# Performance work log

Hardware: AMD Instinct MI355X
Metric: run time of the kernel (lower is better)

The kernel has to match this reference:

```python
import jax, jax.numpy as jnp
import numpy as np

B, DIM, H, W = 128, 640, 10, 10
M = H * W


def setup_inputs() -> dict:
    key = jax.random.key(0)
    x = jax.random.normal(key, (B, DIM, M), dtype=jnp.float32)
    # learned temperature parameter, init = log(1 / (2*h*w)), shape (1, 1)
    t = jnp.log(1.0 / (2 * H * W) * jnp.ones((1, 1), dtype=jnp.float32))
    return {"x": x, "t": t}


def reference(x, t):
    # x: [B, dim, M], t: [1, 1] temperature (log-scale)
    dim = x.shape[1]
    # Gram matrix x x^T: [B, dim, dim]
    xxT = jnp.einsum('bdm,bem->bde', x, x)
    # I_M.bmm(x_pow2*I) and (x_pow2*I).bmm(I_M) are just diagonal broadcasts
    d = jnp.diagonal(xxT, axis1=1, axis2=2)  # [B, dim]
    dcov = d[:, None, :] + d[:, :, None] - 2.0 * xxT
    dcov = jnp.maximum(dcov, 1e-4)
    dcov = jnp.sqrt(jnp.exp(t) * dcov + 1e-5)
    # double centering: dcov.bmm(I_M)/dim == row means, I_M.bmm(dcov)/dim == col means
    row_mean = jnp.mean(dcov, axis=2, keepdims=True)   # [B, dim, 1]
    col_mean = jnp.mean(dcov, axis=1, keepdims=True)   # [B, 1, dim]
    tot_mean = jnp.mean(dcov, axis=(1, 2), keepdims=True)  # [B, 1, 1]
    out = dcov - row_mean - col_mean + tot_mean
    return out.reshape(out.shape[0], dim * dim)
```

## Files before the change

### kernel.cpp

```cpp
#include <hip/hip_runtime.h>
#include <cmath>

#define NB    128
#define DIM_  640
#define MM    100
#define LDK   136
#define TS    72
#define TTS   68

#define NWG   (NB * 55)
#define CPX   (NWG / 8)

typedef _Float16 half8 __attribute__((ext_vector_type(8)));
typedef _Float16 half4_t __attribute__((ext_vector_type(4)));
typedef float f32x4 __attribute__((ext_vector_type(4)));

__device__ inline void decode_bp(int bid, int& b, int& p) {
    const int dec = (bid & 7) * CPX + (bid >> 3);
    b = dec / 55;
    p = dec - b * 55;
}

__device__ inline void stage_tile_d(const float* __restrict__ src,
                                    _Float16* __restrict__ lds,
                                    float* __restrict__ dsrow, int tid) {
    const int row = tid >> 2;
    const int sub = tid & 3;
    const float* sr = src + (size_t)row * MM + sub * 4;
    _Float16* lr = lds + row * LDK + sub * 4;
    float acc = 0.f;
    #pragma unroll
    for (int k = 0; k < 6; ++k) {
        const float4 v = *(const float4*)(sr + 16 * k);
        half4_t h;
        h.x = (_Float16)v.x; h.y = (_Float16)v.y;
        h.z = (_Float16)v.z; h.w = (_Float16)v.w;
        *(half4_t*)(lr + 16 * k) = h;
        const float a0 = (float)h.x, a1 = (float)h.y,
                    a2 = (float)h.z, a3 = (float)h.w;
        acc += a0 * a0 + a1 * a1 + a2 * a2 + a3 * a3;
    }
    if (sub == 0) {
        const float4 v = *(const float4*)(sr + 96);
        half4_t h;
        h.x = (_Float16)v.x; h.y = (_Float16)v.y;
        h.z = (_Float16)v.z; h.w = (_Float16)v.w;
        *(half4_t*)(lr + 96) = h;
        const float a0 = (float)h.x, a1 = (float)h.y,
                    a2 = (float)h.z, a3 = (float)h.w;
        acc += a0 * a0 + a1 * a1 + a2 * a2 + a3 * a3;
    }
    acc += __shfl_xor(acc, 1, 64);
    acc += __shfl_xor(acc, 2, 64);
    if (sub == 0) dsrow[row] = acc;
    const float2 z2 = make_float2(0.f, 0.f);
    for (int i = tid; i < 64 * 7; i += 256) {
        const int r = i / 7;
        const int c = 100 + (i - r * 7) * 4;
        *(float2*)(&lds[r * LDK + c]) = z2;
    }
}

__global__ __launch_bounds__(256) void bdc_pass1(
        const float* __restrict__ x, const float* __restrict__ t,
        float* __restrict__ r2, _Float16* __restrict__ dc) {
    __shared__ alignas(16) _Float16 As[64 * LDK];
    __shared__ alignas(16) _Float16 Bs[64 * LDK];
    __shared__ float rowacc[64];
    __shared__ float colacc[64];
    __shared__ float dsi[64];
    __shared__ float dsj[64];
    _Float16* T = As;

    int b, p;
    decode_bp(blockIdx.x, b, p);
    int it = 0, rem = p;
    while (rem >= 10 - it) { rem -= 10 - it; ++it; }
    const int jt = it + rem;
    const bool diag = (it == jt);

    const int tid = threadIdx.x;
    const int wave = tid >> 6;
    const int lane = tid & 63;
    const int l16  = lane & 15;
    const int quad = lane >> 4;
    const int rowhalf = wave >> 1;
    const int colhalf = wave & 1;

    if (tid < 64)  rowacc[tid] = 0.f;
    else if (tid < 128) colacc[tid - 64] = 0.f;

    const float* xb = x + (size_t)b * DIM_ * MM;
    stage_tile_d(xb + (size_t)(it * 64) * MM, As, dsi, tid);
    if (!diag) stage_tile_d(xb + (size_t)(jt * 64) * MM, Bs, dsj, tid);

    const float expt = expf(t[0]);

    __syncthreads();

    const float* dsjp = diag ? dsi : dsj;
    float dr[2][4];
    #pragma unroll
    for (int ti = 0; ti < 2; ++ti)
        #pragma unroll
        for (int r = 0; r < 4; ++r)
            dr[ti][r] = dsi[rowhalf * 32 + ti * 16 + quad * 4 + r];
    const float dcv[2] = { dsjp[colhalf * 32 + l16], dsjp[colhalf * 32 + 16 + l16] };

    const int rbase = it * 64 + rowhalf * 32;
    const int cbase = jt * 64 + colhalf * 32;

    const _Float16* Bp = diag ? As : Bs;
    f32x4 acc[2][2] = {};
    #pragma unroll
    for (int kk = 0; kk < 4; ++kk) {
        const int k = kk * 32 + quad * 8;
        half8 a0 = *(const half8*)(&As[(rowhalf * 32 + l16) * LDK + k]);
        half8 a1 = *(const half8*)(&As[(rowhalf * 32 + 16 + l16) * LDK + k]);
        half8 b0 = *(const half8*)(&Bp[(colhalf * 32 + l16) * LDK + k]);
        half8 b1 = *(const half8*)(&Bp[(colhalf * 32 + 16 + l16) * LDK + k]);
        acc[0][0] = __builtin_amdgcn_mfma_f32_16x16x32_f16(a0, b0, acc[0][0], 0, 0, 0);
        acc[0][1] = __builtin_amdgcn_mfma_f32_16x16x32_f16(a0, b1, acc[0][1], 0, 0, 0);
        acc[1][0] = __builtin_amdgcn_mfma_f32_16x16x32_f16(a1, b0, acc[1][0], 0, 0, 0);
        acc[1][1] = __builtin_amdgcn_mfma_f32_16x16x32_f16(a1, b1, acc[1][1], 0, 0, 0);
    }

    float v[2][4][2];
    float cp0 = 0.f, cp1 = 0.f;
    #pragma unroll
    for (int ti = 0; ti < 2; ++ti) {
        #pragma unroll
        for (int r = 0; r < 4; ++r) {
            const int gi = rbase + ti * 16 + quad * 4 + r;
            #pragma unroll
            for (int tj = 0; tj < 2; ++tj) {
                const int gj = cbase + tj * 16 + l16;
                float raw = dr[ti][r] + dcv[tj] - 2.0f * acc[ti][tj][r];
                raw = (gi == gj) ? 1e-4f : fmaxf(raw, 1e-4f);
                v[ti][r][tj] = sqrtf(expt * raw + 1e-5f);
            }
            cp0 += v[ti][r][0];
            cp1 += v[ti][r][1];
            float s = v[ti][r][0] + v[ti][r][1];
            s += __shfl_xor(s, 1, 64);
            s += __shfl_xor(s, 2, 64);
            s += __shfl_xor(s, 4, 64);
            s += __shfl_xor(s, 8, 64);
            if (l16 == 0)
                atomicAdd(&rowacc[rowhalf * 32 + ti * 16 + quad * 4 + r], s);
        }
    }
    cp0 += __shfl_xor(cp0, 16, 64); cp0 += __shfl_xor(cp0, 32, 64);
    cp1 += __shfl_xor(cp1, 16, 64); cp1 += __shfl_xor(cp1, 32, 64);
    if (quad == 0) {
        atomicAdd(&colacc[colhalf * 32 + l16],      cp0);
        atomicAdd(&colacc[colhalf * 32 + 16 + l16], cp1);
    }

    __syncthreads();

    #pragma unroll
    for (int ti = 0; ti < 2; ++ti)
        #pragma unroll
        for (int r = 0; r < 4; ++r) {
            const int ri = rowhalf * 32 + ti * 16 + quad * 4 + r;
            T[ri * TS + colhalf * 32 + l16]      = (_Float16)v[ti][r][0];
            T[ri * TS + colhalf * 32 + 16 + l16] = (_Float16)v[ti][r][1];
        }

    __syncthreads();

    _Float16* dcT = dc + ((size_t)(b * 55 + p)) * 4096;
    #pragma unroll
    for (int w = tid; w < 512; w += 256) {
        const int r2i = w >> 3;
        const int c2  = (w & 7) * 8;
        *(half8*)(dcT + r2i * 64 + c2) = *(const half8*)(&T[r2i * TS + c2]);
    }

    if (tid < 64) {
        r2[((size_t)b * 10 + jt) * DIM_ + it * 64 + tid] = rowacc[tid];
        if (!diag)
            r2[((size_t)b * 10 + it) * DIM_ + jt * 64 + tid] = colacc[tid];
    }
}

__global__ __launch_bounds__(256) void bdc_center(
        const _Float16* __restrict__ dc, const float* __restrict__ r2,
        float* __restrict__ out) {
    __shared__ alignas(16) float Tt[64 * TTS];
    __shared__ float rm_s[DIM_];
    __shared__ float wred[4];

    int b, p;
    decode_bp(blockIdx.x, b, p);
    int it = 0, rem = p;
    while (rem >= 10 - it) { rem -= 10 - it; ++it; }
    const int jt = it + rem;
    const bool diag = (it == jt);

    const int tid  = threadIdx.x;
    const int lane = tid & 63;
    const int wave = tid >> 6;

    const float* rb = r2 + (size_t)b * 10 * DIM_;
    float tpart = 0.f;
    for (int i = tid; i < DIM_; i += 256) {
        float s = 0.f;
        #pragma unroll
        for (int ss = 0; ss < 10; ++ss) s += rb[ss * DIM_ + i];
        rm_s[i] = s * (1.0f / 640.0f);
        tpart += s;
    }
    #pragma unroll
    for (int off = 32; off; off >>= 1) tpart += __shfl_xor(tpart, off, 64);
    if (lane == 0) wred[wave] = tpart;
    __syncthreads();
    const float tot = (wred[0] + wred[1] + wred[2] + wred[3]) * (1.0f / 409600.0f);

    const _Float16* dcT = dc + ((size_t)(b * 55 + p)) * 4096;
    float* ob = out + (size_t)b * DIM_ * DIM_;

    #pragma unroll
    for (int k2 = 0; k2 < 2; ++k2) {
        const int w  = tid + k2 * 256;
        const int r  = w >> 3;
        const int c8 = (w & 7) * 8;
        const half8 h = *(const half8*)(dcT + r * 64 + c8);
        const float ci = tot - rm_s[it * 64 + r];
        float o[8];
        #pragma unroll
        for (int k = 0; k < 8; ++k)
            o[k] = (float)h[k] - rm_s[jt * 64 + c8 + k] + ci;
        f32x4 o0 = { o[0], o[1], o[2], o[3] };
        f32x4 o1 = { o[4], o[5], o[6], o[7] };
        f32x4* op = (f32x4*)(ob + (size_t)(it * 64 + r) * DIM_ + jt * 64 + c8);
        op[0] = o0; op[1] = o1;
        if (!diag) {
            #pragma unroll
            for (int k = 0; k < 8; ++k)
                Tt[(c8 + k) * TTS + r] = o[k];
        }
    }

    if (!diag) {
        __syncthreads();
        #pragma unroll
        for (int k4 = 0; k4 < 4; ++k4) {
            const int u  = tid + k4 * 256;
            const int rr = u >> 4;
            const int c4 = (u & 15) * 4;
            const f32x4 vv = *(const f32x4*)(&Tt[rr * TTS + c4]);
            *(f32x4*)(ob + (size_t)(jt * 64 + rr) * DIM_ + it * 64 + c4) = vv;
        }
    }
}

extern "C" void kernel_launch(void* const* d_in, const int* in_sizes, int n_in,
                              void* d_out, int out_size, void* d_ws, size_t ws_size,
                              hipStream_t stream) {
    const float* x = (const float*)d_in[0];
    const float* t = (const float*)d_in[1];
    float* out = (float*)d_out;

    char* ws = (char*)d_ws;
    float*    r2 = (float*)ws;
    _Float16* dc = (_Float16*)(ws + 3276800);

    bdc_pass1<<<dim3(NWG), dim3(256), 0, stream>>>(x, t, r2, dc);
    bdc_center<<<dim3(NWG), dim3(256), 0, stream>>>(dc, r2, out);
}
```

Baseline: 289.5 us.

## Recompute Gram tiles in output pass instead of storing fp16 dcov intermediate

Adds a prep kernel that converts x to padded fp16 rows and computes squared norms once. The first pass then only produces row/column sums, and the output pass recomputes the MFMA Gram tile and sqrt instead of reading a stored fp16 dcov tile. This drops the round trip of the dcov intermediate through global memory in exchange for a third launch, doubled matmul work, and a swizzled LDS transpose.

```diff
diff --git a/kernel.cpp b/kernel.cpp
--- a/kernel.cpp
+++ b/kernel.cpp
@@ -4,15 +4,15 @@
 #define NB    128
 #define DIM_  640
 #define MM    100
+#define XHR   128
 #define LDK   136
-#define TS    72
-#define TTS   68
+#define TFS   68
+#define TTS   66
 
 #define NWG   (NB * 55)
 #define CPX   (NWG / 8)
 
 typedef _Float16 half8 __attribute__((ext_vector_type(8)));
-typedef _Float16 half4_t __attribute__((ext_vector_type(4)));
 typedef float f32x4 __attribute__((ext_vector_type(4)));
 
 __device__ inline void decode_bp(int bid, int& b, int& p) {
@@ -21,56 +21,43 @@
     p = dec - b * 55;
 }
 
-__device__ inline void stage_tile_d(const float* __restrict__ src,
-                                    _Float16* __restrict__ lds,
-                                    float* __restrict__ dsrow, int tid) {
-    const int row = tid >> 2;
-    const int sub = tid & 3;
-    const float* sr = src + (size_t)row * MM + sub * 4;
-    _Float16* lr = lds + row * LDK + sub * 4;
-    float acc = 0.f;
-    #pragma unroll
-    for (int k = 0; k < 6; ++k) {
-        const float4 v = *(const float4*)(sr + 16 * k);
-        half4_t h;
-        h.x = (_Float16)v.x; h.y = (_Float16)v.y;
-        h.z = (_Float16)v.z; h.w = (_Float16)v.w;
-        *(half4_t*)(lr + 16 * k) = h;
-        const float a0 = (float)h.x, a1 = (float)h.y,
-                    a2 = (float)h.z, a3 = (float)h.w;
-        acc += a0 * a0 + a1 * a1 + a2 * a2 + a3 * a3;
-    }
-    if (sub == 0) {
-        const float4 v = *(const float4*)(sr + 96);
-        half4_t h;
-        h.x = (_Float16)v.x; h.y = (_Float16)v.y;
-        h.z = (_Float16)v.z; h.w = (_Float16)v.w;
-        *(half4_t*)(lr + 96) = h;
-        const float a0 = (float)h.x, a1 = (float)h.y,
-                    a2 = (float)h.z, a3 = (float)h.w;
-        acc += a0 * a0 + a1 * a1 + a2 * a2 + a3 * a3;
-    }
-    acc += __shfl_xor(acc, 1, 64);
-    acc += __shfl_xor(acc, 2, 64);
-    if (sub == 0) dsrow[row] = acc;
-    const float2 z2 = make_float2(0.f, 0.f);
-    for (int i = tid; i < 64 * 7; i += 256) {
-        const int r = i / 7;
-        const int c = 100 + (i - r * 7) * 4;
-        *(float2*)(&lds[r * LDK + c]) = z2;
-    }
-}
-
-__global__ __launch_bounds__(256) void bdc_pass1(
-        const float* __restrict__ x, const float* __restrict__ t,
-        float* __restrict__ r2, _Float16* __restrict__ dc) {
+__global__ __launch_bounds__(256) void prep_xh(const float* __restrict__ x,
+                                               _Float16* __restrict__ xh,
+                                               float* __restrict__ d) {
+    const int row  = blockIdx.x * 4 + (threadIdx.x >> 6);
+    const int lane = threadIdx.x & 63;
+    const float* xr = x + (size_t)row * MM;
+    float2 v = make_float2(0.f, 0.f);
+    if (lane < 50) v = *(const float2*)(xr + 2 * lane);
+    const _Float16 h0 = (_Float16)v.x, h1 = (_Float16)v.y;
+    const float a0 = (float)h0, a1 = (float)h1;
+    float acc = a0 * a0 + a1 * a1;
+    union { _Float16 h[2]; unsigned u; } pk;
+    pk.h[0] = h0; pk.h[1] = h1;
+    *(unsigned*)(xh + (size_t)row * XHR + 2 * lane) = pk.u;
+    #pragma unroll
+    for (int off = 32; off; off >>= 1) acc += __shfl_down(acc, off, 64);
+    if (lane == 0) d[row] = acc;
+}
+
+__device__ inline void stage_xh(const _Float16* __restrict__ src,
+                                _Float16* __restrict__ lds, int tid) {
+    #pragma unroll
+    for (int i = 0; i < 4; ++i) {
+        const int idx = tid + i * 256;
+        const int row = idx >> 4;
+        const int m   = idx & 15;
+        *(half8*)(lds + row * LDK + m * 8) = *(const half8*)(src + (size_t)row * XHR + m * 8);
+    }
+}
+
+__global__ __launch_bounds__(256) void bdc_sums(
+        const _Float16* __restrict__ xh, const float* __restrict__ d,
+        const float* __restrict__ t, float* __restrict__ r2) {
     __shared__ alignas(16) _Float16 As[64 * LDK];
     __shared__ alignas(16) _Float16 Bs[64 * LDK];
     __shared__ float rowacc[64];
     __shared__ float colacc[64];
-    __shared__ float dsi[64];
-    __shared__ float dsj[64];
-    _Float16* T = As;
 
     int b, p;
     decode_bp(blockIdx.x, b, p);
@@ -90,25 +77,23 @@
     if (tid < 64)  rowacc[tid] = 0.f;
     else if (tid < 128) colacc[tid - 64] = 0.f;
 
-    const float* xb = x + (size_t)b * DIM_ * MM;
-    stage_tile_d(xb + (size_t)(it * 64) * MM, As, dsi, tid);
-    if (!diag) stage_tile_d(xb + (size_t)(jt * 64) * MM, Bs, dsj, tid);
+    const _Float16* xb = xh + (size_t)b * DIM_ * XHR;
+    stage_xh(xb + (size_t)(it * 64) * XHR, As, tid);
+    if (!diag) stage_xh(xb + (size_t)(jt * 64) * XHR, Bs, tid);
 
     const float expt = expf(t[0]);
-
-    __syncthreads();
-
-    const float* dsjp = diag ? dsi : dsj;
-    float dr[2][4];
-    #pragma unroll
-    for (int ti = 0; ti < 2; ++ti)
-        #pragma unroll
-        for (int r = 0; r < 4; ++r)
-            dr[ti][r] = dsi[rowhalf * 32 + ti * 16 + quad * 4 + r];
-    const float dcv[2] = { dsjp[colhalf * 32 + l16], dsjp[colhalf * 32 + 16 + l16] };
-
+    const float* db = d + b * DIM_;
     const int rbase = it * 64 + rowhalf * 32;
     const int cbase = jt * 64 + colhalf * 32;
+    float dr[2][4];
+    #pragma unroll
+    for (int ti = 0; ti < 2; ++ti)
+        #pragma unroll
+        for (int r = 0; r < 4; ++r)
+            dr[ti][r] = db[rbase + ti * 16 + quad * 4 + r];
+    const float dcv[2] = { db[cbase + l16], db[cbase + 16 + l16] };
+
+    __syncthreads();
 
     const _Float16* Bp = diag ? As : Bs;
     f32x4 acc[2][2] = {};
@@ -125,23 +110,20 @@
         acc[1][1] = __builtin_amdgcn_mfma_f32_16x16x32_f16(a1, b1, acc[1][1], 0, 0, 0);
     }
 
-    float v[2][4][2];
     float cp0 = 0.f, cp1 = 0.f;
     #pragma unroll
     for (int ti = 0; ti < 2; ++ti) {
         #pragma unroll
         for (int r = 0; r < 4; ++r) {
             const int gi = rbase + ti * 16 + quad * 4 + r;
-            #pragma unroll
-            for (int tj = 0; tj < 2; ++tj) {
-                const int gj = cbase + tj * 16 + l16;
-                float raw = dr[ti][r] + dcv[tj] - 2.0f * acc[ti][tj][r];
-                raw = (gi == gj) ? 1e-4f : fmaxf(raw, 1e-4f);
-                v[ti][r][tj] = sqrtf(expt * raw + 1e-5f);
-            }
-            cp0 += v[ti][r][0];
-            cp1 += v[ti][r][1];
-            float s = v[ti][r][0] + v[ti][r][1];
+            float raw0 = dr[ti][r] + dcv[0] - 2.0f * acc[ti][0][r];
+            raw0 = (gi == cbase + l16) ? 1e-4f : fmaxf(raw0, 1e-4f);
+            const float v0 = sqrtf(expt * raw0 + 1e-5f);
+            float raw1 = dr[ti][r] + dcv[1] - 2.0f * acc[ti][1][r];
+            raw1 = (gi == cbase + 16 + l16) ? 1e-4f : fmaxf(raw1, 1e-4f);
+            const float v1 = sqrtf(expt * raw1 + 1e-5f);
+            cp0 += v0; cp1 += v1;
+            float s = v0 + v1;
             s += __shfl_xor(s, 1, 64);
             s += __shfl_xor(s, 2, 64);
             s += __shfl_xor(s, 4, 64);
@@ -159,25 +141,6 @@
 
     __syncthreads();
 
-    #pragma unroll
-    for (int ti = 0; ti < 2; ++ti)
-        #pragma unroll
-        for (int r = 0; r < 4; ++r) {
-            const int ri = rowhalf * 32 + ti * 16 + quad * 4 + r;
-            T[ri * TS + colhalf * 32 + l16]      = (_Float16)v[ti][r][0];
-            T[ri * TS + colhalf * 32 + 16 + l16] = (_Float16)v[ti][r][1];
-        }
-
-    __syncthreads();
-
-    _Float16* dcT = dc + ((size_t)(b * 55 + p)) * 4096;
-    #pragma unroll
-    for (int w = tid; w < 512; w += 256) {
-        const int r2i = w >> 3;
-        const int c2  = (w & 7) * 8;
-        *(half8*)(dcT + r2i * 64 + c2) = *(const half8*)(&T[r2i * TS + c2]);
-    }
-
     if (tid < 64) {
         r2[((size_t)b * 10 + jt) * DIM_ + it * 64 + tid] = rowacc[tid];
         if (!diag)
@@ -185,10 +148,15 @@
     }
 }
 
-__global__ __launch_bounds__(256) void bdc_center(
-        const _Float16* __restrict__ dc, const float* __restrict__ r2,
+__global__ __launch_bounds__(256) void bdc_out(
+        const _Float16* __restrict__ xh, const float* __restrict__ d,
+        const float* __restrict__ t, const float* __restrict__ r2,
         float* __restrict__ out) {
-    __shared__ alignas(16) float Tt[64 * TTS];
+    __shared__ alignas(16) char uni[35200];
+    _Float16* As = (_Float16*)uni;
+    _Float16* Bs = (_Float16*)(uni + 17408);
+    float* Tf = (float*)uni;
+    float* Tt = (float*)(uni + 17408);
     __shared__ float rm_s[DIM_];
     __shared__ float wred[4];
 
@@ -200,8 +168,16 @@
     const bool diag = (it == jt);
 
     const int tid  = threadIdx.x;
+    const int wave = tid >> 6;
     const int lane = tid & 63;
-    const int wave = tid >> 6;
+    const int l16  = lane & 15;
+    const int quad = lane >> 4;
+    const int rowhalf = wave >> 1;
+    const int colhalf = wave & 1;
+
+    const _Float16* xb = xh + (size_t)b * DIM_ * XHR;
+    stage_xh(xb + (size_t)(it * 64) * XHR, As, tid);
+    if (!diag) stage_xh(xb + (size_t)(jt * 64) * XHR, Bs, tid);
 
     const float* rb = r2 + (size_t)b * 10 * DIM_;
     float tpart = 0.f;
@@ -215,43 +191,91 @@
     #pragma unroll
     for (int off = 32; off; off >>= 1) tpart += __shfl_xor(tpart, off, 64);
     if (lane == 0) wred[wave] = tpart;
+
+    const float expt = expf(t[0]);
+    const float* db = d + b * DIM_;
+    const int rbase = it * 64 + rowhalf * 32;
+    const int cbase = jt * 64 + colhalf * 32;
+    float dr[2][4];
+    #pragma unroll
+    for (int ti = 0; ti < 2; ++ti)
+        #pragma unroll
+        for (int r = 0; r < 4; ++r)
+            dr[ti][r] = db[rbase + ti * 16 + quad * 4 + r];
+    const float dcv[2] = { db[cbase + l16], db[cbase + 16 + l16] };
+
     __syncthreads();
     const float tot = (wred[0] + wred[1] + wred[2] + wred[3]) * (1.0f / 409600.0f);
 
-    const _Float16* dcT = dc + ((size_t)(b * 55 + p)) * 4096;
+    const _Float16* Bp = diag ? As : Bs;
+    f32x4 acc[2][2] = {};
+    #pragma unroll
+    for (int kk = 0; kk < 4; ++kk) {
+        const int k = kk * 32 + quad * 8;
+        half8 a0 = *(const half8*)(&As[(rowhalf * 32 + l16) * LDK + k]);
+        half8 a1 = *(const half8*)(&As[(rowhalf * 32 + 16 + l16) * LDK + k]);
+        half8 b0 = *(const half8*)(&Bp[(colhalf * 32 + l16) * LDK + k]);
+        half8 b1 = *(const half8*)(&Bp[(colhalf * 32 + 16 + l16) * LDK + k]);
+        acc[0][0] = __builtin_amdgcn_mfma_f32_16x16x32_f16(a0, b0, acc[0][0], 0, 0, 0);
+        acc[0][1] = __builtin_amdgcn_mfma_f32_16x16x32_f16(a0, b1, acc[0][1], 0, 0, 0);
+        acc[1][0] = __builtin_amdgcn_mfma_f32_16x16x32_f16(a1, b0, acc[1][0], 0, 0, 0);
+        acc[1][1] = __builtin_amdgcn_mfma_f32_16x16x32_f16(a1, b1, acc[1][1], 0, 0, 0);
+    }
+
+    float o[2][4][2];
+    #pragma unroll
+    for (int ti = 0; ti < 2; ++ti)
+        #pragma unroll
+        for (int r = 0; r < 4; ++r) {
+            const int gi = rbase + ti * 16 + quad * 4 + r;
+            const float rowterm = tot - rm_s[gi];
+            #pragma unroll
+            for (int tj = 0; tj < 2; ++tj) {
+                const int gj = cbase + tj * 16 + l16;
+                float raw = dr[ti][r] + dcv[tj] - 2.0f * acc[ti][tj][r];
+                raw = (gi == gj) ? 1e-4f : fmaxf(raw, 1e-4f);
+                o[ti][r][tj] = sqrtf(expt * raw + 1e-5f) + rowterm - rm_s[gj];
+            }
+        }
+
+    __syncthreads();
+
+    #pragma unroll
+    for (int ti = 0; ti < 2; ++ti)
+        #pragma unroll
+        for (int r = 0; r < 4; ++r) {
+            const int rowl = rowhalf * 32 + ti * 16 + quad * 4 + r;
+            #pragma unroll
+            for (int tj = 0; tj < 2; ++tj) {
+                const int coll = colhalf * 32 + tj * 16 + l16;
+                Tf[rowl * TFS + coll] = o[ti][r][tj];
+                if (!diag)
+                    Tt[coll * TTS + (rowl ^ ((l16 & 3) << 2))] = o[ti][r][tj];
+            }
+        }
+
+    __syncthreads();
+
     float* ob = out + (size_t)b * DIM_ * DIM_;
-
-    #pragma unroll
-    for (int k2 = 0; k2 < 2; ++k2) {
-        const int w  = tid + k2 * 256;
-        const int r  = w >> 3;
-        const int c8 = (w & 7) * 8;
-        const half8 h = *(const half8*)(dcT + r * 64 + c8);
-        const float ci = tot - rm_s[it * 64 + r];
-        float o[8];
-        #pragma unroll
-        for (int k = 0; k < 8; ++k)
-            o[k] = (float)h[k] - rm_s[jt * 64 + c8 + k] + ci;
-        f32x4 o0 = { o[0], o[1], o[2], o[3] };
-        f32x4 o1 = { o[4], o[5], o[6], o[7] };
-        f32x4* op = (f32x4*)(ob + (size_t)(it * 64 + r) * DIM_ + jt * 64 + c8);
-        op[0] = o0; op[1] = o1;
-        if (!diag) {
-            #pragma unroll
-            for (int k = 0; k < 8; ++k)
-                Tt[(c8 + k) * TTS + r] = o[k];
-        }
-    }
-
+    #pragma unroll
+    for (int k4 = 0; k4 < 4; ++k4) {
+        const int w  = tid + k4 * 256;
+        const int rr = w >> 4;
+        const int c4 = (w & 15) * 4;
+        const f32x4 v = *(const f32x4*)(&Tf[rr * TFS + c4]);
+        *(f32x4*)(ob + (size_t)(it * 64 + rr) * DIM_ + jt * 64 + c4) = v;
+    }
     if (!diag) {
-        __syncthreads();
         #pragma unroll
         for (int k4 = 0; k4 < 4; ++k4) {
-            const int u  = tid + k4 * 256;
-            const int rr = u >> 4;
-            const int c4 = (u & 15) * 4;
-            const f32x4 vv = *(const f32x4*)(&Tt[rr * TTS + c4]);
-            *(f32x4*)(ob + (size_t)(jt * 64 + rr) * DIM_ + it * 64 + c4) = vv;
+            const int w  = tid + k4 * 256;
+            const int rr = w >> 4;
+            const int c4 = (w & 15) * 4;
+            const int cc = c4 ^ ((rr & 3) << 2);
+            const float2 p0 = *(const float2*)(&Tt[rr * TTS + cc]);
+            const float2 p1 = *(const float2*)(&Tt[rr * TTS + cc + 2]);
+            const f32x4 v = { p0.x, p0.y, p1.x, p1.y };
+            *(f32x4*)(ob + (size_t)(jt * 64 + rr) * DIM_ + it * 64 + c4) = v;
         }
     }
 }
@@ -264,9 +288,11 @@
     float* out = (float*)d_out;
 
     char* ws = (char*)d_ws;
-    float*    r2 = (float*)ws;
-    _Float16* dc = (_Float16*)(ws + 3276800);
-
-    bdc_pass1<<<dim3(NWG), dim3(256), 0, stream>>>(x, t, r2, dc);
-    bdc_center<<<dim3(NWG), dim3(256), 0, stream>>>(dc, r2, out);
-}
+    _Float16* xh = (_Float16*)ws;
+    float*    d  = (float*)(ws + 20971520);
+    float*    r2 = (float*)(ws + 20971520 + 327680);
+
+    prep_xh<<<dim3(NB * DIM_ / 4), dim3(256), 0, stream>>>(x, xh, d);
+    bdc_sums<<<dim3(NWG), dim3(256), 0, stream>>>(xh, d, t, r2);
+    bdc_out<<<dim3(NWG), dim3(256), 0, stream>>>(xh, d, t, r2, out);
+}
```

Result: faster. 283.5 us (-2.1%).
